# Kernel optimization log

Hardware: AMD Instinct MI355X
Metric: run time of the kernel (lower is better)

The kernel has to match this reference:

```python
import jax, jax.numpy as jnp
import numpy as np

N_NODES = 100000
N_EDGES = 1600000
N_GRAPHS = 512
NUM_REL = 3


def setup_inputs() -> dict:
    key = jax.random.key(0)
    ks = jax.random.split(key, 16)
    shape_idx = jax.random.randint(ks[0], (N_NODES,), 0, 16)
    color_idx = jax.random.randint(ks[1], (N_NODES,), 0, 8)
    node_feats = jnp.stack([shape_idx, color_idx], axis=1)  # [N,2] int
    edge_index = jax.random.randint(ks[2], (2, N_EDGES), 0, N_NODES)
    edge_type = jax.random.randint(ks[3], (N_EDGES,), 0, NUM_REL)
    batch = jnp.sort(jax.random.randint(ks[4], (N_NODES,), 0, N_GRAPHS))
    s = lambda k, sh: jax.random.normal(k, sh, dtype=jnp.float32) * 0.05
    return {
        'node_feats': node_feats,
        'edge_index': edge_index,
        'edge_type': edge_type,
        'batch': batch,
        'shape_emb': s(ks[5], (16, 8)),
        'color_emb': s(ks[6], (8, 8)),
        'pre_w': s(ks[7], (16, 32)),
        'pre_b': jnp.zeros((32,), jnp.float32),
        'root1': s(ks[8], (32, 64)),
        'rel1': s(ks[9], (NUM_REL, 32, 64)),
        'bias1': jnp.zeros((64,), jnp.float32),
        'root2': s(ks[10], (64, 64)),
        'rel2': s(ks[11], (NUM_REL, 64, 64)),
        'bias2': jnp.zeros((64,), jnp.float32),
        'cls_w': s(ks[12], (64, 10)),
        'cls_b': jnp.zeros((10,), jnp.float32),
    }


def rgcn_conv(x, edge_index, edge_type, root, rel_w, bias):
    # PyG RGCNConv: out_i = x_i @ root + sum_r mean_{j in N_r(i)} x_j @ W_r + bias
    src, dst = edge_index[0], edge_index[1]
    out = x @ root + bias
    xs = x[src]  # [E, in] gathered source features
    for r in range(NUM_REL):
        m = (edge_type == r).astype(x.dtype)  # [E]
        msg = (xs @ rel_w[r]) * m[:, None]  # [E, out]
        agg = jax.ops.segment_sum(msg, dst, num_segments=N_NODES)
        cnt = jax.ops.segment_sum(m, dst, num_segments=N_NODES)
        out = out + agg / jnp.maximum(cnt, 1.0)[:, None]
    return out


def reference(node_feats, edge_index, edge_type, batch, shape_emb, color_emb,
              pre_w, pre_b, root1, rel1, bias1, root2, rel2, bias2, cls_w, cls_b):
    x = jnp.concatenate([shape_emb[node_feats[:, 0]], color_emb[node_feats[:, 1]]], axis=1)  # [N,16]
    x = jax.nn.relu(x @ pre_w + pre_b)  # [N,32]
    x = jax.nn.relu(rgcn_conv(x, edge_index, edge_type, root1, rel1, bias1))  # [N,64]
    x = jax.nn.relu(rgcn_conv(x, edge_index, edge_type, root2, rel2, bias2))  # [N,64]
    # global_mean_pool over graph ids
    s = jax.ops.segment_sum(x, batch, num_segments=N_GRAPHS)
    c = jax.ops.segment_sum(jnp.ones((x.shape[0],), x.dtype), batch, num_segments=N_GRAPHS)
    pooled = s / jnp.maximum(c, 1.0)[:, None]  # [G,64]
    return pooled @ cls_w + cls_b  # [G,num_classes]
```

## Files before the change

kernel.cpp:

```cpp
#include <hip/hip_runtime.h>

#define NN 100000
#define NE 1600000
#define NG 512

#define BSH 9
#define NB 196
#define EPB 8192
#define NAB ((NE + EPB - 1) / EPB)
#define CAPB 9216
#define CAP 9216

__global__ __launch_bounds__(256) void k_embed(
    const int* __restrict__ nf, const float* __restrict__ semb,
    const float* __restrict__ cemb, const float* __restrict__ pw,
    const float* __restrict__ pb, float* __restrict__ x1)
{
  int gid = blockIdx.x * 256 + threadIdx.x;
  bool valid = gid < NN;
  int i = valid ? gid : NN - 1;
  int sf = nf[2 * i], cf = nf[2 * i + 1];
  float x0[16];
#pragma unroll
  for (int k = 0; k < 8; ++k) x0[k] = semb[sf * 8 + k];
#pragma unroll
  for (int k = 0; k < 8; ++k) x0[8 + k] = cemb[cf * 8 + k];
  float acc[32];
#pragma unroll
  for (int j = 0; j < 32; ++j) acc[j] = pb[j];
#pragma unroll
  for (int k = 0; k < 16; ++k) {
    float xv = x0[k];
#pragma unroll
    for (int j = 0; j < 32; ++j) acc[j] += xv * pw[k * 32 + j];
  }
  if (valid) {
    float4* o = (float4*)(x1 + (size_t)i * 32);
#pragma unroll
    for (int j4 = 0; j4 < 8; ++j4) {
      float4 v;
      v.x = fmaxf(acc[4 * j4 + 0], 0.f);
      v.y = fmaxf(acc[4 * j4 + 1], 0.f);
      v.z = fmaxf(acc[4 * j4 + 2], 0.f);
      v.w = fmaxf(acc[4 * j4 + 3], 0.f);
      o[j4] = v;
    }
  }
}


__global__ __launch_bounds__(256) void kA_scatter(
    const int* __restrict__ ei, const int* __restrict__ et,
    int* __restrict__ bkt_cur, int* __restrict__ binned)
{
  __shared__ int packA[EPB];
  __shared__ unsigned char bktA[EPB];
  __shared__ int lh[NB], grun[NB], lcur[NB];
  for (int b = threadIdx.x; b < NB; b += 256) { lh[b] = 0; lcur[b] = 0; }
  __syncthreads();
  int base = blockIdx.x * EPB;
#pragma unroll
  for (int i = 0; i < EPB / 256; ++i) {
    int p = i * 256 + threadIdx.x;
    int e = base + p;
    if (e < NE) {
      int src = ei[e], dst = ei[NE + e], ty = et[e];
      int b = dst >> BSH;
      packA[p] = src | (ty << 17) | ((dst & 511) << 19);
      bktA[p] = (unsigned char)b;
      atomicAdd(&lh[b], 1);
    } else {
      bktA[p] = 255;
    }
  }
  __syncthreads();
  for (int b = threadIdx.x; b < NB; b += 256)
    grun[b] = lh[b] ? atomicAdd(&bkt_cur[b], lh[b]) : 0;
  __syncthreads();
#pragma unroll
  for (int i = 0; i < EPB / 256; ++i) {
    int p = i * 256 + threadIdx.x;
    int b = bktA[p];
    if (b != 255) {
      int off = grun[b] + atomicAdd(&lcur[b], 1);
      if (off < CAPB) binned[b * CAPB + off] = packA[p];
    }
  }
}

__global__ __launch_bounds__(512) void kB_build(
    const int* __restrict__ bkt_cur, const int* __restrict__ binned,
    int* __restrict__ rs4, int* __restrict__ ep)
{
  __shared__ int stage[CAP];
  __shared__ int ldeg3[1536], lrs3[1536], lcur3[1536];
  __shared__ int sm[2][512];
  int b = blockIdx.x;
  int t = threadIdx.x;
  int p0 = b * CAPB;
  int cnt = bkt_cur[b];
  if (cnt > CAPB) cnt = CAPB;
  int nodes0 = b << BSH;
  int nnodes = NN - nodes0 < 512 ? NN - nodes0 : 512;
  ldeg3[t] = 0; ldeg3[t + 512] = 0; ldeg3[t + 1024] = 0;
  lcur3[t] = 0; lcur3[t + 512] = 0; lcur3[t + 1024] = 0;
  __syncthreads();
  for (int p = t; p < cnt; p += 512) {
    int pk = binned[p0 + p];
    if (p < CAP) stage[p] = pk;
    int key = ((pk >> 19) & 511) * 3 + ((pk >> 17) & 3);
    atomicAdd(&ldeg3[key], 1);
  }
  __syncthreads();
  int s0 = ldeg3[3 * t], s1 = ldeg3[3 * t + 1], s2 = ldeg3[3 * t + 2];
  int tot = s0 + s1 + s2;
  sm[0][t] = tot;
  __syncthreads();
  int cur = 0;
#pragma unroll
  for (int off = 1; off < 512; off <<= 1) {
    int add = (t >= off) ? sm[cur][t - off] : 0;
    sm[cur ^ 1][t] = sm[cur][t] + add;
    __syncthreads();
    cur ^= 1;
  }
  int ex = sm[cur][t] - tot;
  int r0 = p0 + ex, r1 = r0 + s0, r2 = r1 + s1;
  lrs3[3 * t] = r0;
  lrs3[3 * t + 1] = r1;
  lrs3[3 * t + 2] = r2;
  if (t < nnodes) {
    *(int4*)(rs4 + (size_t)4 * (nodes0 + t)) = make_int4(r0, r1, r2, r2 + s2);
  }
  __syncthreads();
  for (int p = t; p < cnt; p += 512) {
    int pk = (p < CAP) ? stage[p] : binned[p0 + p];
    int key = ((pk >> 19) & 511) * 3 + ((pk >> 17) & 3);
    int off = atomicAdd(&lcur3[key], 1);
    ep[lrs3[key] + off] = pk & 0x1FFFF;
  }
}

template <int IN>
__global__ __launch_bounds__(512) void k_fused(
    const float* __restrict__ x, const int* __restrict__ rs4,
    const int* __restrict__ ep, const float* __restrict__ root,
    const float* __restrict__ rel, const float* __restrict__ bias,
    float* __restrict__ y)
{
  __shared__ float smem[3 * IN][65];
  const int tid = threadIdx.x;
  const int node0 = blockIdx.x * 64;
  const int wv = tid >> 6;
  const int lane = tid & 63;

  constexpr int LPE = IN / 4;
  constexpr int DPW = (IN == 32) ? 2 : 1;
  constexpr int SW = 64 / DPW;
  constexpr int EPI = SW / LPE;
  const int sub = (IN == 64) ? 0 : (lane >> 5);
  const int sl = lane & (SW - 1);
  const int k4 = sl % LPE;
  const int es = sl / LPE;
  const int subBase = lane & ~(SW - 1);

  for (int it = 0; it < 8 / DPW; ++it) {
    int dl = wv * 8 + it * DPW + sub;
    int d = node0 + dl;
    int4 q = make_int4(0, 0, 0, 0);
    if (d < NN) q = *(const int4*)(rs4 + (size_t)4 * d);
    const int q0 = q.x, q1 = q.y, q2 = q.z, q3 = q.w;
    float4 a0 = make_float4(0.f, 0.f, 0.f, 0.f);
    float4 a1 = make_float4(0.f, 0.f, 0.f, 0.f);
    float4 a2 = make_float4(0.f, 0.f, 0.f, 0.f);
    for (int base = q0; base < q3; base += SW) {
      int epv = ep[base + sl];
      int pend = (base + SW < q3) ? base + SW : q3;
#pragma unroll 4
      for (int p = base; p < pend; p += EPI) {
        int idx = p + es;
        bool val = idx < pend;
        int srcLane = subBase | ((idx - base) & (SW - 1));
        int e = __shfl(epv, srcLane, 64);
        float4 v = *(const float4*)(x + (size_t)e * IN + k4 * 4);
        float m0 = (val && idx < q1) ? 1.f : 0.f;
        float m1 = (val && idx >= q1 && idx < q2) ? 1.f : 0.f;
        float m2 = (val && idx >= q2) ? 1.f : 0.f;
        a0.x = fmaf(m0, v.x, a0.x); a0.y = fmaf(m0, v.y, a0.y);
        a0.z = fmaf(m0, v.z, a0.z); a0.w = fmaf(m0, v.w, a0.w);
        a1.x = fmaf(m1, v.x, a1.x); a1.y = fmaf(m1, v.y, a1.y);
        a1.z = fmaf(m1, v.z, a1.z); a1.w = fmaf(m1, v.w, a1.w);
        a2.x = fmaf(m2, v.x, a2.x); a2.y = fmaf(m2, v.y, a2.y);
        a2.z = fmaf(m2, v.z, a2.z); a2.w = fmaf(m2, v.w, a2.w);
      }
    }
#pragma unroll
    for (int off = LPE; off < SW; off <<= 1) {
      a0.x += __shfl_xor(a0.x, off, 64); a0.y += __shfl_xor(a0.y, off, 64);
      a0.z += __shfl_xor(a0.z, off, 64); a0.w += __shfl_xor(a0.w, off, 64);
      a1.x += __shfl_xor(a1.x, off, 64); a1.y += __shfl_xor(a1.y, off, 64);
      a1.z += __shfl_xor(a1.z, off, 64); a1.w += __shfl_xor(a1.w, off, 64);
      a2.x += __shfl_xor(a2.x, off, 64); a2.y += __shfl_xor(a2.y, off, 64);
      a2.z += __shfl_xor(a2.z, off, 64); a2.w += __shfl_xor(a2.w, off, 64);
    }
    if (es == 0) {
      float c0 = (float)(q1 - q0 > 0 ? q1 - q0 : 1);
      float c1 = (float)(q2 - q1 > 0 ? q2 - q1 : 1);
      float c2 = (float)(q3 - q2 > 0 ? q3 - q2 : 1);
      int r0 = k4 * 4;
      smem[0 * IN + r0 + 0][dl] = a0.x / c0;
      smem[0 * IN + r0 + 1][dl] = a0.y / c0;
      smem[0 * IN + r0 + 2][dl] = a0.z / c0;
      smem[0 * IN + r0 + 3][dl] = a0.w / c0;
      smem[1 * IN + r0 + 0][dl] = a1.x / c1;
      smem[1 * IN + r0 + 1][dl] = a1.y / c1;
      smem[1 * IN + r0 + 2][dl] = a1.z / c1;
      smem[1 * IN + r0 + 3][dl] = a1.w / c1;
      smem[2 * IN + r0 + 0][dl] = a2.x / c2;
      smem[2 * IN + r0 + 1][dl] = a2.y / c2;
      smem[2 * IN + r0 + 2][dl] = a2.z / c2;
      smem[2 * IN + r0 + 3][dl] = a2.w / c2;
    }
  }
  __syncthreads();

  const int n = lane;
  const int j0 = __builtin_amdgcn_readfirstlane(wv * 8);
  constexpr int F4 = IN / 4;
  constexpr int NPF = (64 * F4) / 512;

  float4 pf[NPF];
#pragma unroll
  for (int u = 0; u < NPF; ++u) {
    int idx = u * 512 + tid;
    int nn = idx / F4, c4 = idx % F4;
    int node = node0 + nn;
    pf[u] = make_float4(0.f, 0.f, 0.f, 0.f);
    if (node < NN) pf[u] = *(const float4*)(x + (size_t)node * IN + c4 * 4);
  }

  float acc[8];
#pragma unroll
  for (int j = 0; j < 8; ++j) acc[j] = bias[j0 + j];

  auto mm = [&](const float* __restrict__ W, int row0) {
#pragma unroll 4
    for (int k = 0; k < IN; ++k) {
      float sk = smem[row0 + k][n];
      const float* w = W + (size_t)k * 64 + j0;
#pragma unroll
      for (int j = 0; j < 8; ++j) acc[j] = fmaf(sk, w[j], acc[j]);
    }
  };

  mm(rel, 0);
  mm(rel + (size_t)IN * 64, IN);
  mm(rel + (size_t)2 * IN * 64, 2 * IN);
  __syncthreads();

#pragma unroll
  for (int u = 0; u < NPF; ++u) {
    int idx = u * 512 + tid;
    int nn = idx / F4, c4 = idx % F4;
    smem[c4 * 4 + 0][nn] = pf[u].x;
    smem[c4 * 4 + 1][nn] = pf[u].y;
    smem[c4 * 4 + 2][nn] = pf[u].z;
    smem[c4 * 4 + 3][nn] = pf[u].w;
  }
  __syncthreads();
  mm(root, 0);

  int node = node0 + n;
  if (node < NN) {
    float4* o = (float4*)(y + (size_t)node * 64 + j0);
    float4 v;
    v.x = fmaxf(acc[0], 0.f); v.y = fmaxf(acc[1], 0.f);
    v.z = fmaxf(acc[2], 0.f); v.w = fmaxf(acc[3], 0.f);
    o[0] = v;
    v.x = fmaxf(acc[4], 0.f); v.y = fmaxf(acc[5], 0.f);
    v.z = fmaxf(acc[6], 0.f); v.w = fmaxf(acc[7], 0.f);
    o[1] = v;
  }
}

__global__ __launch_bounds__(256) void k_pool(
    const float* __restrict__ x3, const int* __restrict__ batch,
    float* __restrict__ pooled, float* __restrict__ gcnt)
{
  int gwave = (blockIdx.x * 256 + threadIdx.x) >> 6;
  int lane = threadIdx.x & 63;
  int n0 = gwave * 64;
  if (n0 >= NN) return;
  int n1 = n0 + 64 < NN ? n0 + 64 : NN;
  int gcur = batch[n0];
  float acc = 0.f;
  int run = 0;
  for (int n = n0; n < n1; ++n) {
    int g = batch[n];
    if (g != gcur) {
      atomicAdd(&pooled[gcur * 64 + lane], acc);
      if (lane == 0) atomicAdd(&gcnt[gcur], (float)run);
      acc = 0.f; run = 0; gcur = g;
    }
    acc += x3[(size_t)n * 64 + lane];
    ++run;
  }
  atomicAdd(&pooled[gcur * 64 + lane], acc);
  if (lane == 0) atomicAdd(&gcnt[gcur], (float)run);
}

__global__ __launch_bounds__(256) void k_cls(
    const float* __restrict__ pooled, const float* __restrict__ gcnt,
    const float* __restrict__ cw, const float* __restrict__ cb, float* __restrict__ out)
{
  int t = blockIdx.x * 256 + threadIdx.x;
  if (t >= NG * 10) return;
  int g = t / 10, c = t % 10;
  float cf = fmaxf(gcnt[g], 1.f);
  float acc = cb[c];
#pragma unroll 8
  for (int k = 0; k < 64; ++k)
    acc += (pooled[g * 64 + k] / cf) * cw[k * 10 + c];
  out[t] = acc;
}

extern "C" void kernel_launch(void* const* d_in, const int* in_sizes, int n_in,
                              void* d_out, int out_size, void* d_ws, size_t ws_size,
                              hipStream_t stream)
{
  const int* nf = (const int*)d_in[0];
  const int* ei = (const int*)d_in[1];
  const int* et = (const int*)d_in[2];
  const int* batch = (const int*)d_in[3];
  const float* semb = (const float*)d_in[4];
  const float* cemb = (const float*)d_in[5];
  const float* pw = (const float*)d_in[6];
  const float* pb = (const float*)d_in[7];
  const float* root1 = (const float*)d_in[8];
  const float* rel1 = (const float*)d_in[9];
  const float* bias1 = (const float*)d_in[10];
  const float* root2 = (const float*)d_in[11];
  const float* rel2 = (const float*)d_in[12];
  const float* bias2 = (const float*)d_in[13];
  const float* cw = (const float*)d_in[14];
  const float* cb = (const float*)d_in[15];
  float* out = (float*)d_out;

  char* ws = (char*)d_ws;
  size_t off = 0;
  auto alloc = [&](size_t bytes) {
    char* p = ws + off;
    off += (bytes + 255) & ~(size_t)255;
    return p;
  };
  int* bkt_cur = (int*)alloc((size_t)NB * 4);
  int* rs4 = (int*)alloc((size_t)NN * 4 * 4);
  int* ep = (int*)alloc(((size_t)NB * CAPB + 64) * 4);
  int* binned = (int*)alloc((size_t)NB * CAPB * 4);
  float* xA = (float*)alloc((size_t)NN * 64 * 4);
  float* xB = (float*)alloc((size_t)NN * 64 * 4);
  float* pooled = (float*)alloc((size_t)NG * 64 * 4);
  float* gcnt = (float*)alloc((size_t)NG * 4);
  (void)ws_size; (void)in_sizes; (void)n_in; (void)out_size;

  hipMemsetAsync(bkt_cur, 0, (size_t)NB * 4, stream);
  hipMemsetAsync(ep, 0, ((size_t)NB * CAPB + 64) * 4, stream);
  k_embed<<<(NN + 255) / 256, 256, 0, stream>>>(nf, semb, cemb, pw, pb, xB);

  kA_scatter<<<NAB, 256, 0, stream>>>(ei, et, bkt_cur, binned);
  kB_build<<<NB, 512, 0, stream>>>(bkt_cur, binned, rs4, ep);

  int fgrid = (NN + 63) / 64;

  k_fused<32><<<fgrid, 512, 0, stream>>>(xB, rs4, ep, root1, rel1, bias1, xA);
  k_fused<64><<<fgrid, 512, 0, stream>>>(xA, rs4, ep, root2, rel2, bias2, xB);

  hipMemsetAsync(pooled, 0, (size_t)NG * 64 * 4, stream);
  hipMemsetAsync(gcnt, 0, (size_t)NG * 4, stream);
  int nwaves = (NN + 63) / 64;
  k_pool<<<(nwaves + 3) / 4, 256, 0, stream>>>(xB, batch, pooled, gcnt);
  k_cls<<<(NG * 10 + 255) / 256, 256, 0, stream>>>(pooled, gcnt, cw, cb, out);
}
```

Baseline: 287.4 us.

## Shrink fused RGCN shared memory by spilling third relation aggregate to global

The fused RGCN kernel now keeps only two relation aggregates in LDS and writes the third relation's mean aggregate to a global scratch buffer. It later reloads that buffer, transposes it into LDS, and runs the third relation's matmul, then loads x for the root matmul. The point is to cut LDS per block from 3*IN to 2*IN rows, and the launch bounds now request 8 waves-per-EU, both to allow more resident blocks. The cost is an extra global write and read of an N x IN buffer, two more barriers, and possible register pressure from the tighter launch bound.

```diff
diff --git a/kernel.cpp b/kernel.cpp
--- a/kernel.cpp
+++ b/kernel.cpp
@@ -47,7 +47,6 @@
     }
   }
 }
-
 
 __global__ __launch_bounds__(256) void kA_scatter(
     const int* __restrict__ ei, const int* __restrict__ et,
@@ -142,13 +141,13 @@
 }
 
 template <int IN>
-__global__ __launch_bounds__(512) void k_fused(
+__global__ __launch_bounds__(512, 8) void k_fused(
     const float* __restrict__ x, const int* __restrict__ rs4,
     const int* __restrict__ ep, const float* __restrict__ root,
     const float* __restrict__ rel, const float* __restrict__ bias,
-    float* __restrict__ y)
-{
-  __shared__ float smem[3 * IN][65];
+    float* __restrict__ h2, float* __restrict__ y)
+{
+  __shared__ float smem[2 * IN][65];
   const int tid = threadIdx.x;
   const int node0 = blockIdx.x * 64;
   const int wv = tid >> 6;
@@ -203,7 +202,7 @@
       a2.x += __shfl_xor(a2.x, off, 64); a2.y += __shfl_xor(a2.y, off, 64);
       a2.z += __shfl_xor(a2.z, off, 64); a2.w += __shfl_xor(a2.w, off, 64);
     }
-    if (es == 0) {
+    if (es == 0 && d < NN) {
       float c0 = (float)(q1 - q0 > 0 ? q1 - q0 : 1);
       float c1 = (float)(q2 - q1 > 0 ? q2 - q1 : 1);
       float c2 = (float)(q3 - q2 > 0 ? q3 - q2 : 1);
@@ -216,10 +215,9 @@
       smem[1 * IN + r0 + 1][dl] = a1.y / c1;
       smem[1 * IN + r0 + 2][dl] = a1.z / c1;
       smem[1 * IN + r0 + 3][dl] = a1.w / c1;
-      smem[2 * IN + r0 + 0][dl] = a2.x / c2;
-      smem[2 * IN + r0 + 1][dl] = a2.y / c2;
-      smem[2 * IN + r0 + 2][dl] = a2.z / c2;
-      smem[2 * IN + r0 + 3][dl] = a2.w / c2;
+      float4 o2;
+      o2.x = a2.x / c2; o2.y = a2.y / c2; o2.z = a2.z / c2; o2.w = a2.w / c2;
+      *(float4*)(h2 + (size_t)d * IN + r0) = o2;
     }
   }
   __syncthreads();
@@ -230,13 +228,15 @@
   constexpr int NPF = (64 * F4) / 512;
 
   float4 pf[NPF];
+  int s_nn[NPF], s_c4[NPF];
 #pragma unroll
   for (int u = 0; u < NPF; ++u) {
     int idx = u * 512 + tid;
-    int nn = idx / F4, c4 = idx % F4;
-    int node = node0 + nn;
+    s_nn[u] = idx / F4;
+    s_c4[u] = idx % F4;
+    int node = node0 + s_nn[u];
     pf[u] = make_float4(0.f, 0.f, 0.f, 0.f);
-    if (node < NN) pf[u] = *(const float4*)(x + (size_t)node * IN + c4 * 4);
+    if (node < NN) pf[u] = *(const float4*)(h2 + (size_t)node * IN + s_c4[u] * 4);
   }
 
   float acc[8];
@@ -255,20 +255,36 @@
 
   mm(rel, 0);
   mm(rel + (size_t)IN * 64, IN);
-  mm(rel + (size_t)2 * IN * 64, 2 * IN);
   __syncthreads();
 
 #pragma unroll
   for (int u = 0; u < NPF; ++u) {
-    int idx = u * 512 + tid;
-    int nn = idx / F4, c4 = idx % F4;
+    int c4 = s_c4[u], nn = s_nn[u];
     smem[c4 * 4 + 0][nn] = pf[u].x;
     smem[c4 * 4 + 1][nn] = pf[u].y;
     smem[c4 * 4 + 2][nn] = pf[u].z;
     smem[c4 * 4 + 3][nn] = pf[u].w;
   }
-  __syncthreads();
-  mm(root, 0);
+#pragma unroll
+  for (int u = 0; u < NPF; ++u) {
+    int node = node0 + s_nn[u];
+    pf[u] = make_float4(0.f, 0.f, 0.f, 0.f);
+    if (node < NN) pf[u] = *(const float4*)(x + (size_t)node * IN + s_c4[u] * 4);
+  }
+  __syncthreads();
+  mm(rel + (size_t)2 * IN * 64, 0);
+  __syncthreads();
+
+#pragma unroll
+  for (int u = 0; u < NPF; ++u) {
+    int c4 = s_c4[u], nn = s_nn[u];
+    smem[IN + c4 * 4 + 0][nn] = pf[u].x;
+    smem[IN + c4 * 4 + 1][nn] = pf[u].y;
+    smem[IN + c4 * 4 + 2][nn] = pf[u].z;
+    smem[IN + c4 * 4 + 3][nn] = pf[u].w;
+  }
+  __syncthreads();
+  mm(root, IN);
 
   int node = node0 + n;
   if (node < NN) {
@@ -357,6 +373,7 @@
   int* rs4 = (int*)alloc((size_t)NN * 4 * 4);
   int* ep = (int*)alloc(((size_t)NB * CAPB + 64) * 4);
   int* binned = (int*)alloc((size_t)NB * CAPB * 4);
+  float* h2 = (float*)alloc((size_t)NN * 64 * 4);
   float* xA = (float*)alloc((size_t)NN * 64 * 4);
   float* xB = (float*)alloc((size_t)NN * 64 * 4);
   float* pooled = (float*)alloc((size_t)NG * 64 * 4);
@@ -372,8 +389,8 @@
 
   int fgrid = (NN + 63) / 64;
 
-  k_fused<32><<<fgrid, 512, 0, stream>>>(xB, rs4, ep, root1, rel1, bias1, xA);
-  k_fused<64><<<fgrid, 512, 0, stream>>>(xA, rs4, ep, root2, rel2, bias2, xB);
+  k_fused<32><<<fgrid, 512, 0, stream>>>(xB, rs4, ep, root1, rel1, bias1, h2, xA);
+  k_fused<64><<<fgrid, 512, 0, stream>>>(xA, rs4, ep, root2, rel2, bias2, h2, xB);
 
   hipMemsetAsync(pooled, 0, (size_t)NG * 64 * 4, stream);
   hipMemsetAsync(gcnt, 0, (size_t)NG * 4, stream);
```

After: 267.5 us. -6.9%, faster.
